# Kernel optimization log

Hardware: AMD Instinct MI355X
Metric: run time of the kernel (lower is better)

Reference implementation:

```python
import jax, jax.numpy as jnp
import numpy as np

VOCAB, EMB, HID = 5000, 16, 32


def setup_inputs() -> dict:
    key = jax.random.key(0)
    k1, k2, k3, k4 = jax.random.split(key, 4)
    B, T = 512, 2048
    tokens = jax.random.randint(k1, (B, T), 0, VOCAB, dtype=jnp.int32)
    emb_table = jax.random.normal(k2, (VOCAB, EMB), dtype=jnp.float32) * 0.05
    # Keras LSTM weights: kernel [EMB, 4*HID], recurrent_kernel [HID, 4*HID], bias [4*HID]
    kernel = jax.random.normal(k3, (EMB, 4 * HID), dtype=jnp.float32) * (1.0 / np.sqrt(EMB))
    rec_kernel = jax.random.normal(k4, (HID, 4 * HID), dtype=jnp.float32) * (1.0 / np.sqrt(HID))
    # Keras unit_forget_bias default: forget gate bias = 1
    bias = jnp.concatenate([jnp.zeros((HID,)), jnp.ones((HID,)), jnp.zeros((2 * HID,))]).astype(jnp.float32)
    return {"tokens": tokens, "emb_table": emb_table, "kernel": kernel,
            "rec_kernel": rec_kernel, "bias": bias}


def _masked_lstm(x_seq, mask_seq, kernel, rec_kernel, bias):
    # x_seq: [T, B, EMB], mask_seq: [T, B] bool
    T, B, _ = x_seq.shape
    # precompute input projections for all steps: [T, B, 4H]
    xz = jnp.einsum('tbe,eg->tbg', x_seq, kernel) + bias

    def step(carry, inp):
        h, c = carry
        xz_t, m = inp  # [B,4H], [B]
        z = xz_t + h @ rec_kernel
        i, f, g, o = jnp.split(z, 4, axis=-1)  # Keras gate order: i, f, c, o
        i = jax.nn.sigmoid(i); f = jax.nn.sigmoid(f); o = jax.nn.sigmoid(o)
        c_new = f * c + i * jnp.tanh(g)
        h_new = o * jnp.tanh(c_new)
        m = m[:, None]
        h = jnp.where(m, h_new, h)  # masked steps carry state through
        c = jnp.where(m, c_new, c)
        return (h, c), None

    h0 = jnp.zeros((B, HID), dtype=x_seq.dtype)
    c0 = jnp.zeros((B, HID), dtype=x_seq.dtype)
    (h, c), _ = jax.lax.scan(step, (h0, c0), (xz, mask_seq))
    return h  # [B, HID] final output (return_sequences=False)


def reference(tokens, emb_table, kernel, rec_kernel, bias):
    mask = tokens != 0                       # mask_zero=True
    x = emb_table[tokens]                    # [B, T, EMB]
    x_seq = jnp.swapaxes(x, 0, 1)            # [T, B, EMB]
    mask_seq = jnp.swapaxes(mask, 0, 1)      # [T, B]
    return _masked_lstm(x_seq, mask_seq, kernel, rec_kernel, bias)
```

## Files before the change

### kernel.cpp

```cpp
#include <hip/hip_runtime.h>

typedef float v2f __attribute__((ext_vector_type(2)));
typedef int   v2i __attribute__((ext_vector_type(2)));
typedef int   v8i __attribute__((ext_vector_type(8)));

#define VOCABN 5000
#define EMBD   16
#define HIDN   32
#define GATES  128
#define BATCH  512
#define SEQT   2048
#define TB     8
#define NTB    (SEQT / TB)

#define S1f (-1.4426950408889634f)
#define S2f (-2.8853900817779268f)

__device__ __forceinline__ float rcp1p2(float x) {
    return __builtin_amdgcn_rcpf(1.0f + __builtin_amdgcn_exp2f(x));
}

__global__ __launch_bounds__(64, 1) void build_proj_kernel(
    const float* __restrict__ emb, const float* __restrict__ W,
    const float* __restrict__ bias, v2f* __restrict__ proj2)
{
    const int v = blockIdx.x;
    const int l = threadIdx.x;
    const int j = l & 31;
    const int half = l >> 5;
    const int c0 = j + half * 32;
    const int c1 = j + 64 + half * 32;
    const float sc1 = half ? S1f : S2f;

    float e[EMBD];
#pragma unroll
    for (int k = 0; k < EMBD; ++k) e[k] = emb[v * EMBD + k];
    float z0 = bias[c0];
    float z1 = bias[c1];
#pragma unroll
    for (int k = 0; k < EMBD; ++k) {
        z0 = __builtin_fmaf(e[k], W[k * GATES + c0], z0);
        z1 = __builtin_fmaf(e[k], W[k * GATES + c1], z1);
    }
    proj2[(size_t)v * 64 + l] = (v2f){ S1f * z0, sc1 * z1 };
}

__global__ __launch_bounds__(64, 1) void lstm_scan_kernel(
    const int* __restrict__ tokens, const float* __restrict__ rec,
    const v2f* __restrict__ proj2, float* __restrict__ out)
{
    const int b = blockIdx.x;
    const int l = threadIdx.x;
    const int j = l & 31;
    const int half = l >> 5;
    const int c0 = j + half * 32;
    const int c1 = j + 64 + half * 32;
    const float sc1 = half ? S1f : S2f;

    v2f R2[HIDN];
#pragma unroll
    for (int k = 0; k < HIDN; ++k) {
        R2[k] = (v2f){ S1f * rec[k * GATES + c0], sc1 * rec[k * GATES + c1] };
    }

    const int* __restrict__ trow = tokens + (size_t)b * SEQT;

    float cs = 0.0f, hval = 0.0f;

    v8i tokb   = *(const v8i*)(trow);
    v8i tokb_n = *(const v8i*)(trow + TB);

    v2f xz0 = proj2[(size_t)tokb[0] * 64 + l];
    v2f xz1 = proj2[(size_t)tokb[1] * 64 + l];

    for (int tb = 0; tb < NTB; ++tb) {
        const int nb = (tb + 2 < NTB) ? (tb + 2) : (NTB - 1);
        const v8i tokb_nn = *(const v8i*)(trow + nb * TB);

#pragma unroll
        for (int s = 0; s < TB; ++s) {
            const int tpre2 = (s < TB - 2) ? tokb[s + 2] : tokb_n[s - (TB - 2)];
            const v2f xz2 = proj2[(size_t)tpre2 * 64 + l];

            v2f a0 = xz0;
            v2f a1 = (v2f){0.f, 0.f};
            v2f a2 = (v2f){0.f, 0.f};
            v2f a3 = (v2f){0.f, 0.f};
#pragma unroll
            for (int k = 0; k < HIDN; k += 4) {
                const float h0 = __int_as_float(
                    __builtin_amdgcn_readlane(__float_as_int(hval), 32 + k));
                const float h1 = __int_as_float(
                    __builtin_amdgcn_readlane(__float_as_int(hval), 32 + k + 1));
                const float h2 = __int_as_float(
                    __builtin_amdgcn_readlane(__float_as_int(hval), 32 + k + 2));
                const float h3 = __int_as_float(
                    __builtin_amdgcn_readlane(__float_as_int(hval), 32 + k + 3));
                a0 = __builtin_elementwise_fma((v2f){h0, h0}, R2[k],     a0);
                a1 = __builtin_elementwise_fma((v2f){h1, h1}, R2[k + 1], a1);
                a2 = __builtin_elementwise_fma((v2f){h2, h2}, R2[k + 2], a2);
                a3 = __builtin_elementwise_fma((v2f){h3, h3}, R2[k + 3], a3);
            }
            const v2f z = (a0 + a1) + (a2 + a3);

            const float u = rcp1p2(z.x);
            const float w = rcp1p2(z.y);
            const float gg = __builtin_fmaf(2.0f, w, -1.0f);
            const float p = (S2f * u) * gg;

            const v2i pr = __builtin_amdgcn_permlane32_swap(
                __float_as_int(p), __float_as_int(p), false, false);
            const float ps = __int_as_float(pr[0]);

            const float cns = __builtin_fmaf(u, cs, ps);
            const float tc = __builtin_fmaf(2.0f, rcp1p2(cns), -1.0f);
            const float hn = w * tc;

            const bool m = (tokb[s] != 0);
            cs   = m ? cns : cs;
            hval = m ? hn : hval;

            xz0 = xz1; xz1 = xz2;
        }

        tokb = tokb_n;
        tokb_n = tokb_nn;
    }

    if (half) out[(size_t)b * HIDN + j] = hval;
}

extern "C" void kernel_launch(void* const* d_in, const int* in_sizes, int n_in,
                              void* d_out, int out_size, void* d_ws, size_t ws_size,
                              hipStream_t stream)
{
    const int*   tokens = (const int*)d_in[0];
    const float* emb    = (const float*)d_in[1];
    const float* W      = (const float*)d_in[2];
    const float* rec    = (const float*)d_in[3];
    const float* bias   = (const float*)d_in[4];
    float* out = (float*)d_out;
    v2f* proj2 = (v2f*)d_ws;

    hipLaunchKernelGGL(build_proj_kernel, dim3(VOCABN), dim3(64), 0, stream,
                       emb, W, bias, proj2);
    hipLaunchKernelGGL(lstm_scan_kernel, dim3(BATCH), dim3(64), 0, stream,
                       tokens, rec, proj2, out);
}
```

Baseline: 441.9 us.

## Process two batch rows per wavefront to interleave independent LSTM recurrences

```diff
diff --git a/kernel.cpp b/kernel.cpp
--- a/kernel.cpp
+++ b/kernel.cpp
@@ -49,7 +49,8 @@
     const int* __restrict__ tokens, const float* __restrict__ rec,
     const v2f* __restrict__ proj2, float* __restrict__ out)
 {
-    const int b = blockIdx.x;
+    const int bp = blockIdx.x;
+    const int b0 = bp * 2, b1 = bp * 2 + 1;
     const int l = threadIdx.x;
     const int j = l & 31;
     const int half = l >> 5;
@@ -63,71 +64,99 @@
         R2[k] = (v2f){ S1f * rec[k * GATES + c0], sc1 * rec[k * GATES + c1] };
     }
 
-    const int* __restrict__ trow = tokens + (size_t)b * SEQT;
+    const int* __restrict__ trowA = tokens + (size_t)b0 * SEQT;
+    const int* __restrict__ trowB = tokens + (size_t)b1 * SEQT;
 
-    float cs = 0.0f, hval = 0.0f;
+    float csA = 0.0f, hA = 0.0f;
+    float csB = 0.0f, hB = 0.0f;
 
-    v8i tokb   = *(const v8i*)(trow);
-    v8i tokb_n = *(const v8i*)(trow + TB);
+    v8i tokA   = *(const v8i*)(trowA);
+    v8i tokA_n = *(const v8i*)(trowA + TB);
+    v8i tokB   = *(const v8i*)(trowB);
+    v8i tokB_n = *(const v8i*)(trowB + TB);
 
-    v2f xz0 = proj2[(size_t)tokb[0] * 64 + l];
-    v2f xz1 = proj2[(size_t)tokb[1] * 64 + l];
+    v2f xzA0 = proj2[(size_t)tokA[0] * 64 + l];
+    v2f xzB0 = proj2[(size_t)tokB[0] * 64 + l];
+    v2f xzA1 = proj2[(size_t)tokA[1] * 64 + l];
+    v2f xzB1 = proj2[(size_t)tokB[1] * 64 + l];
 
     for (int tb = 0; tb < NTB; ++tb) {
         const int nb = (tb + 2 < NTB) ? (tb + 2) : (NTB - 1);
-        const v8i tokb_nn = *(const v8i*)(trow + nb * TB);
+        const v8i tokA_nn = *(const v8i*)(trowA + nb * TB);
+        const v8i tokB_nn = *(const v8i*)(trowB + nb * TB);
 
 #pragma unroll
         for (int s = 0; s < TB; ++s) {
-            const int tpre2 = (s < TB - 2) ? tokb[s + 2] : tokb_n[s - (TB - 2)];
-            const v2f xz2 = proj2[(size_t)tpre2 * 64 + l];
+            const int tpA = (s < TB - 2) ? tokA[s + 2] : tokA_n[s - (TB - 2)];
+            const int tpB = (s < TB - 2) ? tokB[s + 2] : tokB_n[s - (TB - 2)];
+            const v2f xzA2 = proj2[(size_t)tpA * 64 + l];
+            const v2f xzB2 = proj2[(size_t)tpB * 64 + l];
 
-            v2f a0 = xz0;
-            v2f a1 = (v2f){0.f, 0.f};
-            v2f a2 = (v2f){0.f, 0.f};
-            v2f a3 = (v2f){0.f, 0.f};
+            v2f aA0 = xzA0, aA1 = (v2f){0.f,0.f}, aA2 = (v2f){0.f,0.f}, aA3 = (v2f){0.f,0.f};
+            v2f aB0 = xzB0, aB1 = (v2f){0.f,0.f}, aB2 = (v2f){0.f,0.f}, aB3 = (v2f){0.f,0.f};
 #pragma unroll
             for (int k = 0; k < HIDN; k += 4) {
-                const float h0 = __int_as_float(
-                    __builtin_amdgcn_readlane(__float_as_int(hval), 32 + k));
-                const float h1 = __int_as_float(
-                    __builtin_amdgcn_readlane(__float_as_int(hval), 32 + k + 1));
-                const float h2 = __int_as_float(
-                    __builtin_amdgcn_readlane(__float_as_int(hval), 32 + k + 2));
-                const float h3 = __int_as_float(
-                    __builtin_amdgcn_readlane(__float_as_int(hval), 32 + k + 3));
-                a0 = __builtin_elementwise_fma((v2f){h0, h0}, R2[k],     a0);
-                a1 = __builtin_elementwise_fma((v2f){h1, h1}, R2[k + 1], a1);
-                a2 = __builtin_elementwise_fma((v2f){h2, h2}, R2[k + 2], a2);
-                a3 = __builtin_elementwise_fma((v2f){h3, h3}, R2[k + 3], a3);
+                const float hA0 = __int_as_float(__builtin_amdgcn_readlane(__float_as_int(hA), 32 + k));
+                const float hA1 = __int_as_float(__builtin_amdgcn_readlane(__float_as_int(hA), 32 + k + 1));
+                const float hA2 = __int_as_float(__builtin_amdgcn_readlane(__float_as_int(hA), 32 + k + 2));
+                const float hA3 = __int_as_float(__builtin_amdgcn_readlane(__float_as_int(hA), 32 + k + 3));
+                aA0 = __builtin_elementwise_fma((v2f){hA0, hA0}, R2[k],     aA0);
+                aA1 = __builtin_elementwise_fma((v2f){hA1, hA1}, R2[k + 1], aA1);
+                aA2 = __builtin_elementwise_fma((v2f){hA2, hA2}, R2[k + 2], aA2);
+                aA3 = __builtin_elementwise_fma((v2f){hA3, hA3}, R2[k + 3], aA3);
+                const float hB0 = __int_as_float(__builtin_amdgcn_readlane(__float_as_int(hB), 32 + k));
+                const float hB1 = __int_as_float(__builtin_amdgcn_readlane(__float_as_int(hB), 32 + k + 1));
+                const float hB2 = __int_as_float(__builtin_amdgcn_readlane(__float_as_int(hB), 32 + k + 2));
+                const float hB3 = __int_as_float(__builtin_amdgcn_readlane(__float_as_int(hB), 32 + k + 3));
+                aB0 = __builtin_elementwise_fma((v2f){hB0, hB0}, R2[k],     aB0);
+                aB1 = __builtin_elementwise_fma((v2f){hB1, hB1}, R2[k + 1], aB1);
+                aB2 = __builtin_elementwise_fma((v2f){hB2, hB2}, R2[k + 2], aB2);
+                aB3 = __builtin_elementwise_fma((v2f){hB3, hB3}, R2[k + 3], aB3);
             }
-            const v2f z = (a0 + a1) + (a2 + a3);
+            const v2f zA = (aA0 + aA1) + (aA2 + aA3);
+            const v2f zB = (aB0 + aB1) + (aB2 + aB3);
 
-            const float u = rcp1p2(z.x);
-            const float w = rcp1p2(z.y);
-            const float gg = __builtin_fmaf(2.0f, w, -1.0f);
-            const float p = (S2f * u) * gg;
+            const float uA = rcp1p2(zA.x);
+            const float wA = rcp1p2(zA.y);
+            const float ggA = __builtin_fmaf(2.0f, wA, -1.0f);
+            const float pA = (S2f * uA) * ggA;
+            const v2i prA = __builtin_amdgcn_permlane32_swap(
+                __float_as_int(pA), __float_as_int(pA), false, false);
+            const float psA = __int_as_float(prA[0]);
+            const float cnsA = __builtin_fmaf(uA, csA, psA);
+            const float tcA = __builtin_fmaf(2.0f, rcp1p2(cnsA), -1.0f);
+            const float hnA = wA * tcA;
 
-            const v2i pr = __builtin_amdgcn_permlane32_swap(
-                __float_as_int(p), __float_as_int(p), false, false);
-            const float ps = __int_as_float(pr[0]);
+            const float uB = rcp1p2(zB.x);
+            const float wB = rcp1p2(zB.y);
+            const float ggB = __builtin_fmaf(2.0f, wB, -1.0f);
+            const float pB = (S2f * uB) * ggB;
+            const v2i prB = __builtin_amdgcn_permlane32_swap(
+                __float_as_int(pB), __float_as_int(pB), false, false);
+            const float psB = __int_as_float(prB[0]);
+            const float cnsB = __builtin_fmaf(uB, csB, psB);
+            const float tcB = __builtin_fmaf(2.0f, rcp1p2(cnsB), -1.0f);
+            const float hnB = wB * tcB;
 
-            const float cns = __builtin_fmaf(u, cs, ps);
-            const float tc = __builtin_fmaf(2.0f, rcp1p2(cns), -1.0f);
-            const float hn = w * tc;
+            const bool mA = (tokA[s] != 0);
+            const bool mB = (tokB[s] != 0);
+            csA = mA ? cnsA : csA;
+            hA  = mA ? hnA  : hA;
+            csB = mB ? cnsB : csB;
+            hB  = mB ? hnB  : hB;
 
-            const bool m = (tokb[s] != 0);
-            cs   = m ? cns : cs;
-            hval = m ? hn : hval;
-
-            xz0 = xz1; xz1 = xz2;
+            xzA0 = xzA1; xzA1 = xzA2;
+            xzB0 = xzB1; xzB1 = xzB2;
         }
 
-        tokb = tokb_n;
-        tokb_n = tokb_nn;
+        tokA = tokA_n; tokA_n = tokA_nn;
+        tokB = tokB_n; tokB_n = tokB_nn;
     }
 
-    if (half) out[(size_t)b * HIDN + j] = hval;
+    if (half) {
+        out[(size_t)b0 * HIDN + j] = hA;
+        out[(size_t)b1 * HIDN + j] = hB;
+    }
 }
 
 extern "C" void kernel_launch(void* const* d_in, const int* in_sizes, int n_in,
@@ -144,6 +173,6 @@
 
     hipLaunchKernelGGL(build_proj_kernel, dim3(VOCABN), dim3(64), 0, stream,
                        emb, W, bias, proj2);
-    hipLaunchKernelGGL(lstm_scan_kernel, dim3(BATCH), dim3(64), 0, stream,
+    hipLaunchKernelGGL(lstm_scan_kernel, dim3(BATCH / 2), dim3(64), 0, stream,
                        tokens, rec, proj2, out);
 }
```

Result: slower. 810.9 us (+83.5%).
